# Kernel optimization log

Measured on AMD Instinct MI355X. Metric: run time of the kernel, lower is better.

The kernel has to match this reference:

```python
import jax, jax.numpy as jnp
import numpy as np

N, E = 50000, 800000
IN_F, C, H, OUT_F = 128, 32, 4, 4
HC = H * C
EPS = 1e-5


def gatv2(x, src, dst, ea, Wl, Wr, We, att, bias, concat):
    # x: [N, in], ea: [E, 1], Wl/Wr: [in, H*C], We: [1, H*C], att: [h, C]
    h, c = att.shape
    xl = (x @ Wl).reshape(-1, h, c)          # [N, h, c]
    xr = (x @ Wr).reshape(-1, h, c)          # [N, h, c]
    m = xl[src] + xr[dst] + (ea @ We).reshape(-1, h, c)   # [E, h, c]
    e = jnp.einsum('ehc,hc->eh', jax.nn.leaky_relu(m, 0.2), att)  # [E, h]
    emax = jax.ops.segment_max(e, dst, num_segments=N)
    e = jnp.exp(e - emax[dst])
    denom = jax.ops.segment_sum(e, dst, num_segments=N)
    alpha = e / (denom[dst] + 1e-16)         # [E, h]
    out = jax.ops.segment_sum(alpha[:, :, None] * xl[src], dst, num_segments=N)  # [N, h, c]
    out = out.reshape(N, h * c) if concat else out.mean(axis=1)
    return out + bias


def bn_eval(x, g, b, m, v):
    return (x - m) * jax.lax.rsqrt(v + EPS) * g + b


def setup_inputs() -> dict:
    key = jax.random.key(0)
    ks = iter(jax.random.split(key, 40))
    nrm = lambda shape, s=0.2: jax.random.normal(next(ks), shape, jnp.float32) * s
    d = {}
    d['x'] = jax.random.normal(next(ks), (N, IN_F), jnp.float32)
    d['edge_index'] = jax.random.randint(next(ks), (2, E), 0, N, jnp.int32)
    d['edge_attr'] = jax.random.normal(next(ks), (E, 1), jnp.float32)
    # layer 1
    d['l1_Wl'] = nrm((IN_F, HC)); d['l1_Wr'] = nrm((IN_F, HC))
    d['l1_We'] = nrm((1, HC)); d['l1_att'] = nrm((H, C)); d['l1_b'] = nrm((HC,))
    # layers 2-9 stacked
    d['mid_Wl'] = nrm((8, HC, HC)); d['mid_Wr'] = nrm((8, HC, HC))
    d['mid_We'] = nrm((8, 1, HC)); d['mid_att'] = nrm((8, H, C)); d['mid_b'] = nrm((8, HC))
    # layer 10: heads=1, concat=False
    d['l10_Wl'] = nrm((HC, C)); d['l10_Wr'] = nrm((HC, C))
    d['l10_We'] = nrm((1, C)); d['l10_att'] = nrm((1, C)); d['l10_b'] = nrm((C,))
    # batchnorms (eval mode): bn1-9 stacked, bn10 separate
    d['bn_g'] = jax.random.uniform(next(ks), (9, HC), jnp.float32, 0.5, 1.5)
    d['bn_b'] = nrm((9, HC)); d['bn_m'] = nrm((9, HC))
    d['bn_v'] = jax.random.uniform(next(ks), (9, HC), jnp.float32, 0.5, 1.5)
    d['bn10_g'] = jax.random.uniform(next(ks), (C,), jnp.float32, 0.5, 1.5)
    d['bn10_b'] = nrm((C,)); d['bn10_m'] = nrm((C,))
    d['bn10_v'] = jax.random.uniform(next(ks), (C,), jnp.float32, 0.5, 1.5)
    d['lin_W'] = nrm((C, OUT_F)); d['lin_b'] = nrm((OUT_F,))
    return d


def reference(x, edge_index, edge_attr,
              l1_Wl, l1_Wr, l1_We, l1_att, l1_b,
              mid_Wl, mid_Wr, mid_We, mid_att, mid_b,
              l10_Wl, l10_Wr, l10_We, l10_att, l10_b,
              bn_g, bn_b, bn_m, bn_v,
              bn10_g, bn10_b, bn10_m, bn10_v,
              lin_W, lin_b):
    src, dst = edge_index[0], edge_index[1]
    h = jax.nn.relu(gatv2(x, src, dst, edge_attr, l1_Wl, l1_Wr, l1_We, l1_att, l1_b, True))
    h = bn_eval(h, bn_g[0], bn_b[0], bn_m[0], bn_v[0])
    for i in range(8):  # layers 2-9
        h = jax.nn.relu(gatv2(h, src, dst, edge_attr, mid_Wl[i], mid_Wr[i], mid_We[i], mid_att[i], mid_b[i], True))
        h = bn_eval(h, bn_g[i + 1], bn_b[i + 1], bn_m[i + 1], bn_v[i + 1])
    h = jax.nn.relu(gatv2(h, src, dst, edge_attr, l10_Wl, l10_Wr, l10_We, l10_att, l10_b, False))
    h = bn_eval(h, bn10_g, bn10_b, bn10_m, bn10_v)
    return h @ lin_W + lin_b
```

## Files before the change

kernel.cpp:

```cpp
#include <hip/hip_runtime.h>
#include <math.h>

#define NN 50000
#define EE 800000
#define EPS 1e-5f
#define SCAN_CH 196

#define NEG_BIG (-1e30f)
#define RESCALE_THR 4.0f

#define LO_SCALE 2048.0f
#define LO_INV   (1.0f/2048.0f)

typedef unsigned short u16;
typedef _Float16 f16x8 __attribute__((ext_vector_type(8)));
typedef float f32x4 __attribute__((ext_vector_type(4)));

__device__ __forceinline__ u16 f2h(float f) {
    _Float16 h = (_Float16)f;
    return __builtin_bit_cast(u16, h);
}
__device__ __forceinline__ float h2f(u16 u) {
    return (float)__builtin_bit_cast(_Float16, u);
}

__device__ __forceinline__ float dpp_add8(float x) {
    int t;
    t = __builtin_amdgcn_update_dpp(0, __float_as_int(x), 0xB1, 0xf, 0xf, true);
    x += __int_as_float(t);
    t = __builtin_amdgcn_update_dpp(0, __float_as_int(x), 0x4E, 0xf, 0xf, true);
    x += __int_as_float(t);
    t = __builtin_amdgcn_update_dpp(0, __float_as_int(x), 0x141, 0xf, 0xf, true);
    x += __int_as_float(t);
    return x;
}

__global__ void hist_kernel(const int* __restrict__ dst, int* cnt) {
    int e = blockIdx.x * blockDim.x + threadIdx.x;
    if (e < EE) atomicAdd(&cnt[dst[e]], 1);
}

__global__ void scan_part(const int* __restrict__ cnt, int* __restrict__ part) {
    __shared__ int red[256];
    int b = blockIdx.x, t = threadIdx.x;
    int i = b * SCAN_CH + t;
    int v = (t < SCAN_CH && i < NN) ? cnt[i] : 0;
    red[t] = v;
    __syncthreads();
#pragma unroll
    for (int s = 128; s; s >>= 1) {
        if (t < s) red[t] += red[t + s];
        __syncthreads();
    }
    if (t == 0) part[b] = red[0];
}

__global__ void scan_block(int* part) {
    __shared__ int buf[2][256];
    int t = threadIdx.x;
    int v = part[t];
    int p = 0;
    buf[0][t] = v;
    __syncthreads();
#pragma unroll
    for (int off = 1; off < 256; off <<= 1) {
        buf[p ^ 1][t] = buf[p][t] + ((t >= off) ? buf[p][t - off] : 0);
        __syncthreads();
        p ^= 1;
    }
    part[t] = buf[p][t] - v;
}

__global__ void scan_final(int* __restrict__ cntcur, const int* __restrict__ part,
                           int* __restrict__ row_start) {
    __shared__ int buf[2][256];
    int b = blockIdx.x, t = threadIdx.x;
    int i = b * SCAN_CH + t;
    int v = (t < SCAN_CH && i < NN) ? cntcur[i] : 0;
    int p = 0;
    buf[0][t] = v;
    __syncthreads();
#pragma unroll
    for (int off = 1; off < 256; off <<= 1) {
        buf[p ^ 1][t] = buf[p][t] + ((t >= off) ? buf[p][t - off] : 0);
        __syncthreads();
        p ^= 1;
    }
    if (t < SCAN_CH && i < NN) {
        int pos = part[b] + buf[p][t] - v;
        row_start[i] = pos;
        cntcur[i] = pos;
    }
    if (b == 0 && t == 0) row_start[NN] = EE;
}

__global__ void scatter_kernel(const int* __restrict__ ei, const float* __restrict__ ea,
                               int* cursor, int2* __restrict__ edge_pack) {
    int e = blockIdx.x * blockDim.x + threadIdx.x;
    if (e < EE) {
        int d = ei[EE + e];
        int pos = atomicAdd(&cursor[d], 1);
        edge_pack[pos] = make_int2(ei[e], __float_as_int(ea[e]));
    }
}

__global__ void split_f32(const float* __restrict__ in, u16* __restrict__ hi,
                          u16* __restrict__ lo, int n4) {
    int i = blockIdx.x * blockDim.x + threadIdx.x;
    if (i >= n4) return;
    float4 v = ((const float4*)in)[i];
    ushort4 h, l;
    h.x = f2h(v.x); l.x = f2h((v.x - h2f(h.x)) * LO_SCALE);
    h.y = f2h(v.y); l.y = f2h((v.y - h2f(h.y)) * LO_SCALE);
    h.z = f2h(v.z); l.z = f2h((v.z - h2f(h.z)) * LO_SCALE);
    h.w = f2h(v.w); l.w = f2h((v.w - h2f(h.w)) * LO_SCALE);
    ((ushort4*)hi)[i] = h;
    ((ushort4*)lo)[i] = l;
}

__global__ void conv_w(const float* __restrict__ l1Wl, const float* __restrict__ l1Wr,
                       const float* __restrict__ midWl, const float* __restrict__ midWr,
                       u16* __restrict__ Wh, u16* __restrict__ Wlo) {
    int tid = blockIdx.x * 256 + threadIdx.x;
    if (tid >= 9 * 256 * 128) return;
    int L = tid >> 15;
    int rem = tid & 32767;
    int n = rem >> 7, k = rem & 127;
    const float* WL;
    const float* WR;
    if (L == 0) { WL = l1Wl; WR = l1Wr; }
    else {
        WL = midWl + (size_t)(L - 1) * 16384;
        WR = midWr + (size_t)(L - 1) * 16384;
    }
    float w = (n < 128) ? WL[k * 128 + n] : WR[k * 128 + (n - 128)];
    u16 h = f2h(w);
    Wh[tid] = h;
    Wlo[tid] = f2h((w - h2f(h)) * LO_SCALE);
}

__global__ void conv_w10(const float* __restrict__ Wl, const float* __restrict__ Wr,
                         u16* __restrict__ Wh, u16* __restrict__ Wlo) {
    int tid = blockIdx.x * 256 + threadIdx.x;
    if (tid >= 64 * 128) return;
    int n = tid >> 7, k = tid & 127;
    float w = (n < 32) ? Wl[k * 32 + n] : Wr[k * 32 + (n - 32)];
    u16 h = f2h(w);
    Wh[tid] = h;
    Wlo[tid] = f2h((w - h2f(h)) * LO_SCALE);
}

__global__ __launch_bounds__(256) void gemm_mfma(const u16* __restrict__ Ah,
                                                 const u16* __restrict__ Al,
                                                 const u16* __restrict__ Bh,
                                                 const u16* __restrict__ Bl,
                                                 float* __restrict__ C) {
    int bid = blockIdx.x;
    int jj = bid & 7;
    int y  = (bid >> 3) & 1;
    int x  = (bid >> 4) * 8 + jj;
    if (x >= (NN + 63) / 64) return;

    int w    = threadIdx.x >> 6;
    int lane = threadIdx.x & 63;
    int lr = lane & 15;
    int kg = lane >> 4;
    int rowbase = x * 64;
    int colb = w * 32;
    int colbase = y * 128 + colb;

    f16x8 bh[2][4], bl[2][4];
#pragma unroll
    for (int ct = 0; ct < 2; ++ct) {
        size_t boff = (size_t)(colbase + ct * 16 + lr) * 128 + (size_t)(kg * 8);
#pragma unroll
        for (int ks = 0; ks < 4; ++ks) {
            bh[ct][ks] = *(const f16x8*)(Bh + boff + ks * 32);
            bl[ct][ks] = *(const f16x8*)(Bl + boff + ks * 32);
        }
    }

    auto aoff_of = [&](int rt) {
        int arow = rowbase + rt * 16 + lr;
        if (arow >= NN) arow = NN - 1;
        return (size_t)arow * 128 + (size_t)(kg * 8);
    };
    f16x8 ahc[4], alc[4], ahn[4], aln[4];
    {
        size_t ao = aoff_of(0);
#pragma unroll
        for (int ks = 0; ks < 4; ++ks) {
            ahc[ks] = *(const f16x8*)(Ah + ao + ks * 32);
            alc[ks] = *(const f16x8*)(Al + ao + ks * 32);
        }
    }

    float* Cp = C + (size_t)y * ((size_t)NN * 128);

#pragma unroll
    for (int rt = 0; rt < 4; ++rt) {
        if (rt < 3) {
            size_t ao = aoff_of(rt + 1);
#pragma unroll
            for (int ks = 0; ks < 4; ++ks) {
                ahn[ks] = *(const f16x8*)(Ah + ao + ks * 32);
                aln[ks] = *(const f16x8*)(Al + ao + ks * 32);
            }
        }

        f32x4 aH[2], aL[2];
#pragma unroll
        for (int ct = 0; ct < 2; ++ct) {
            aH[ct] = (f32x4){0.f, 0.f, 0.f, 0.f};
            aL[ct] = (f32x4){0.f, 0.f, 0.f, 0.f};
        }
#pragma unroll
        for (int ks = 0; ks < 4; ++ks) {
#pragma unroll
            for (int ct = 0; ct < 2; ++ct) {
                aH[ct] = __builtin_amdgcn_mfma_f32_16x16x32_f16(ahc[ks], bh[ct][ks], aH[ct], 0, 0, 0);
                aL[ct] = __builtin_amdgcn_mfma_f32_16x16x32_f16(alc[ks], bh[ct][ks], aL[ct], 0, 0, 0);
                aL[ct] = __builtin_amdgcn_mfma_f32_16x16x32_f16(ahc[ks], bl[ct][ks], aL[ct], 0, 0, 0);
            }
        }

        int crow0 = rowbase + rt * 16 + kg * 4;
#pragma unroll
        for (int ct = 0; ct < 2; ++ct) {
            float* cp = Cp + (size_t)crow0 * 128 + colb + ct * 16 + lr;
#pragma unroll
            for (int r = 0; r < 4; ++r) {
                if (crow0 + r < NN)
                    cp[(size_t)r * 128] = fmaf(aL[ct][r], LO_INV, aH[ct][r]);
            }
        }

        if (rt < 3) {
#pragma unroll
            for (int ks = 0; ks < 4; ++ks) { ahc[ks] = ahn[ks]; alc[ks] = aln[ks]; }
        }
    }
}

__global__ __launch_bounds__(256) void gemm_mfma_l10(const u16* __restrict__ Ah,
                                                     const u16* __restrict__ Al,
                                                     const u16* __restrict__ Bh,
                                                     const u16* __restrict__ Bl,
                                                     float* __restrict__ C) {
    int w    = threadIdx.x >> 6;
    int lane = threadIdx.x & 63;
    int lr = lane & 15;
    int kg = lane >> 4;
    int rowbase = blockIdx.x * 64;
    int colb = w * 16;

    f16x8 bh[4], bl[4];
    {
        size_t boff = (size_t)(colb + lr) * 128 + (size_t)(kg * 8);
#pragma unroll
        for (int ks = 0; ks < 4; ++ks) {
            bh[ks] = *(const f16x8*)(Bh + boff + ks * 32);
            bl[ks] = *(const f16x8*)(Bl + boff + ks * 32);
        }
    }

    auto aoff_of = [&](int rt) {
        int arow = rowbase + rt * 16 + lr;
        if (arow >= NN) arow = NN - 1;
        return (size_t)arow * 128 + (size_t)(kg * 8);
    };
    f16x8 ahc[4], alc[4], ahn[4], aln[4];
    {
        size_t ao = aoff_of(0);
#pragma unroll
        for (int ks = 0; ks < 4; ++ks) {
            ahc[ks] = *(const f16x8*)(Ah + ao + ks * 32);
            alc[ks] = *(const f16x8*)(Al + ao + ks * 32);
        }
    }

#pragma unroll
    for (int rt = 0; rt < 4; ++rt) {
        if (rt < 3) {
            size_t ao = aoff_of(rt + 1);
#pragma unroll
            for (int ks = 0; ks < 4; ++ks) {
                ahn[ks] = *(const f16x8*)(Ah + ao + ks * 32);
                aln[ks] = *(const f16x8*)(Al + ao + ks * 32);
            }
        }

        f32x4 aH = (f32x4){0.f, 0.f, 0.f, 0.f};
        f32x4 aL = (f32x4){0.f, 0.f, 0.f, 0.f};
#pragma unroll
        for (int ks = 0; ks < 4; ++ks) {
            aH = __builtin_amdgcn_mfma_f32_16x16x32_f16(ahc[ks], bh[ks], aH, 0, 0, 0);
            aL = __builtin_amdgcn_mfma_f32_16x16x32_f16(alc[ks], bh[ks], aL, 0, 0, 0);
            aL = __builtin_amdgcn_mfma_f32_16x16x32_f16(ahc[ks], bl[ks], aL, 0, 0, 0);
        }

        int crow0 = rowbase + rt * 16 + kg * 4;
        float* cp = C + (size_t)crow0 * 64 + colb + lr;
#pragma unroll
        for (int r = 0; r < 4; ++r) {
            if (crow0 + r < NN)
                cp[(size_t)r * 64] = fmaf(aL[r], LO_INV, aH[r]);
        }

        if (rt < 3) {
#pragma unroll
            for (int ks = 0; ks < 4; ++ks) { ahc[ks] = ahn[ks]; alc[ks] = aln[ks]; }
        }
    }
}

__global__ __launch_bounds__(256) void node_agg_128(const float* __restrict__ xlr,
                                                    const int* __restrict__ row_start,
                                                    const int2* __restrict__ epack,
                                                    const float* __restrict__ We,
                                                    const float* __restrict__ att,
                                                    const float* __restrict__ bias,
                                                    const float* __restrict__ bng,
                                                    const float* __restrict__ bnb,
                                                    const float* __restrict__ bnm,
                                                    const float* __restrict__ bnv,
                                                    u16* __restrict__ ahi,
                                                    u16* __restrict__ alo) {
    int node = (blockIdx.x * blockDim.x + threadIdx.x) >> 6;
    int lane = threadIdx.x & 63;
    if (node >= NN) return;
    int half = lane >> 5;
    int c0   = (lane & 31) << 2;

    const float* xlp = xlr;
    const float* xrp = xlr + (size_t)NN * 128;

    const float L2E = 1.44269504f;
    const float4 xr4 = *(const float4*)(xrp + (size_t)node * 128 + c0);
    const float4 we4 = *(const float4*)(We + c0);
    const float4 at4 = *(const float4*)(att + c0);
    float4 a6, a4;
    a6.x = 0.6f * L2E * at4.x; a4.x = 0.4f * L2E * at4.x;
    a6.y = 0.6f * L2E * at4.y; a4.y = 0.4f * L2E * at4.y;
    a6.z = 0.6f * L2E * at4.z; a4.z = 0.4f * L2E * at4.z;
    a6.w = 0.6f * L2E * at4.w; a4.w = 0.4f * L2E * at4.w;

    int beg = row_start[node], end = row_start[node + 1];
    int lastE = end - 1;

    float mx0 = NEG_BIG, sm0 = 0.f;
    float mx1 = NEG_BIG, sm1 = 0.f;
    float4 ac0 = make_float4(0.f, 0.f, 0.f, 0.f);
    float4 ac1 = make_float4(0.f, 0.f, 0.f, 0.f);

    auto score = [&](float eav, const float4& xv) -> float {
        float m0 = xv.x + fmaf(eav, we4.x, xr4.x);
        float m1 = xv.y + fmaf(eav, we4.y, xr4.y);
        float m2 = xv.z + fmaf(eav, we4.z, xr4.z);
        float m3 = xv.w + fmaf(eav, we4.w, xr4.w);
        float p = fmaf(a6.x, m0, a4.x * fabsf(m0));
        p = fmaf(a6.y, m1, fmaf(a4.y, fabsf(m1), p));
        p = fmaf(a6.z, m2, fmaf(a4.z, fabsf(m2), p));
        p = fmaf(a6.w, m3, fmaf(a4.w, fabsf(m3), p));
        return dpp_add8(p);
    };

    auto upd = [&](float& mx, float& sm, float4& ac, float p, const float4& xv) {
        float d = p - mx;
        if (__ballot(d > RESCALE_THR)) {
            float nm = fmaxf(mx, p);
            float sc = exp2f(mx - nm);
            float w  = exp2f(p - nm);
            sm = fmaf(sm, sc, w);
            ac.x = fmaf(ac.x, sc, w * xv.x);
            ac.y = fmaf(ac.y, sc, w * xv.y);
            ac.z = fmaf(ac.z, sc, w * xv.z);
            ac.w = fmaf(ac.w, sc, w * xv.w);
            mx = nm;
        } else {
            float w = exp2f(d);
            sm += w;
            ac.x = fmaf(w, xv.x, ac.x);
            ac.y = fmaf(w, xv.y, ac.y);
            ac.z = fmaf(w, xv.z, ac.z);
            ac.w = fmaf(w, xv.w, ac.w);
        }
    };

    int j = beg;
    for (; j + 3 < end; j += 4) {
        int2 pkA = epack[j + half];
        int2 pkB = epack[j + 2 + half];
        float4 xA = *(const float4*)(xlp + ((size_t)pkA.x << 7) + c0);
        float4 xB = *(const float4*)(xlp + ((size_t)pkB.x << 7) + c0);
        float pA = score(__int_as_float(pkA.y), xA);
        float pB = score(__int_as_float(pkB.y), xB);
        upd(mx0, sm0, ac0, pA, xA);
        upd(mx1, sm1, ac1, pB, xB);
    }
    if (j < end) {
        int jeA = j + half;       bool dA = jeA > lastE; if (dA) jeA = lastE;
        int jeB = j + 2 + half;   bool dB = jeB > lastE; if (dB) jeB = lastE;
        int2 pkA = epack[jeA];
        int2 pkB = epack[jeB];
        float4 xA = *(const float4*)(xlp + ((size_t)pkA.x << 7) + c0);
        float4 xB = *(const float4*)(xlp + ((size_t)pkB.x << 7) + c0);
        float pA = score(__int_as_float(pkA.y), xA);
        float pB = score(__int_as_float(pkB.y), xB);
        pA = dA ? NEG_BIG : pA;
        pB = dB ? NEG_BIG : pB;
        upd(mx0, sm0, ac0, pA, xA);
        upd(mx1, sm1, ac1, pB, xB);
    }

    float Mx = fmaxf(mx0, mx1);
    float s0 = exp2f(mx0 - Mx), s1 = exp2f(mx1 - Mx);
    float sm = fmaf(sm0, s0, sm1 * s1);
    float4 ac;
    ac.x = fmaf(ac0.x, s0, ac1.x * s1);
    ac.y = fmaf(ac0.y, s0, ac1.y * s1);
    ac.z = fmaf(ac0.z, s0, ac1.z * s1);
    ac.w = fmaf(ac0.w, s0, ac1.w * s1);

    float  Mo  = __shfl_xor(Mx, 32);
    float  smo = __shfl_xor(sm, 32);
    float4 aco;
    aco.x = __shfl_xor(ac.x, 32);
    aco.y = __shfl_xor(ac.y, 32);
    aco.z = __shfl_xor(ac.z, 32);
    aco.w = __shfl_xor(ac.w, 32);
    float Mn = fmaxf(Mx, Mo);
    float ss = exp2f(Mx - Mn), so = exp2f(Mo - Mn);
    sm   = fmaf(sm, ss, smo * so);
    ac.x = fmaf(ac.x, ss, aco.x * so);
    ac.y = fmaf(ac.y, ss, aco.y * so);
    ac.z = fmaf(ac.z, ss, aco.z * so);
    ac.w = fmaf(ac.w, ss, aco.w * so);

    if (half == 0) {
        float inv = 1.f / (sm + 1e-16f);
        const float4 b4  = *(const float4*)(bias + c0);
        const float4 g4  = *(const float4*)(bng + c0);
        const float4 bb4 = *(const float4*)(bnb + c0);
        const float4 m4  = *(const float4*)(bnm + c0);
        const float4 v4  = *(const float4*)(bnv + c0);
        float4 y;
        y.x = fmaxf(fmaf(ac.x, inv, b4.x), 0.f);
        y.y = fmaxf(fmaf(ac.y, inv, b4.y), 0.f);
        y.z = fmaxf(fmaf(ac.z, inv, b4.z), 0.f);
        y.w = fmaxf(fmaf(ac.w, inv, b4.w), 0.f);
        y.x = (y.x - m4.x) * rsqrtf(v4.x + EPS) * g4.x + bb4.x;
        y.y = (y.y - m4.y) * rsqrtf(v4.y + EPS) * g4.y + bb4.y;
        y.z = (y.z - m4.z) * rsqrtf(v4.z + EPS) * g4.z + bb4.z;
        y.w = (y.w - m4.w) * rsqrtf(v4.w + EPS) * g4.w + bb4.w;

        ushort4 hh, ll;
        hh.x = f2h(y.x); ll.x = f2h((y.x - h2f(hh.x)) * LO_SCALE);
        hh.y = f2h(y.y); ll.y = f2h((y.y - h2f(hh.y)) * LO_SCALE);
        hh.z = f2h(y.z); ll.z = f2h((y.z - h2f(hh.z)) * LO_SCALE);
        hh.w = f2h(y.w); ll.w = f2h((y.w - h2f(hh.w)) * LO_SCALE);
        *(ushort4*)(ahi + (size_t)node * 128 + c0) = hh;
        *(ushort4*)(alo + (size_t)node * 128 + c0) = ll;
    }
}

__global__ __launch_bounds__(256) void node_agg_l10(const float* __restrict__ xlr,
                                                    const int* __restrict__ row_start,
                                                    const int2* __restrict__ epack,
                                                    const float* __restrict__ We,
                                                    const float* __restrict__ att,
                                                    const float* __restrict__ bias,
                                                    const float* __restrict__ bng,
                                                    const float* __restrict__ bnb,
                                                    const float* __restrict__ bnm,
                                                    const float* __restrict__ bnv,
                                                    const float* __restrict__ linW,
                                                    const float* __restrict__ linb,
                                                    float* __restrict__ out) {
    int n = (blockIdx.x * blockDim.x + threadIdx.x) >> 5;
    if (n >= NN) return;
    int q    = threadIdx.x & 31;
    int slot = q >> 3;
    int c0   = (q & 7) << 2;

    const float L2E = 1.44269504f;
    const float4 xr = *(const float4*)(xlr + (size_t)n * 64 + 32 + c0);
    const float4 we = *(const float4*)(We + c0);
    const float4 at = *(const float4*)(att + c0);
    float4 a6, a4;
    a6.x = 0.6f * L2E * at.x; a4.x = 0.4f * L2E * at.x;
    a6.y = 0.6f * L2E * at.y; a4.y = 0.4f * L2E * at.y;
    a6.z = 0.6f * L2E * at.z; a4.z = 0.4f * L2E * at.z;
    a6.w = 0.6f * L2E * at.w; a4.w = 0.4f * L2E * at.w;

    int beg = row_start[n], end = row_start[n + 1];
    int lastE = end - 1;

    float mx = NEG_BIG, sm = 0.f;
    float4 ac = make_float4(0.f, 0.f, 0.f, 0.f);

    auto score4 = [&](float eav, const float4& xv) -> float {
        float m0 = xv.x + fmaf(eav, we.x, xr.x);
        float m1 = xv.y + fmaf(eav, we.y, xr.y);
        float m2 = xv.z + fmaf(eav, we.z, xr.z);
        float m3 = xv.w + fmaf(eav, we.w, xr.w);
        float p = fmaf(a6.x, m0, a4.x * fabsf(m0));
        p = fmaf(a6.y, m1, fmaf(a4.y, fabsf(m1), p));
        p = fmaf(a6.z, m2, fmaf(a4.z, fabsf(m2), p));
        p = fmaf(a6.w, m3, fmaf(a4.w, fabsf(m3), p));
        return dpp_add8(p);
    };

    auto upd = [&](float p, const float4& xv) {
        float d = p - mx;
        if (__ballot(d > RESCALE_THR)) {
            float nm = fmaxf(mx, p);
            float sc = exp2f(mx - nm);
            float w  = exp2f(p - nm);
            sm = fmaf(sm, sc, w);
            ac.x = fmaf(ac.x, sc, w * xv.x); ac.y = fmaf(ac.y, sc, w * xv.y);
            ac.z = fmaf(ac.z, sc, w * xv.z); ac.w = fmaf(ac.w, sc, w * xv.w);
            mx = nm;
        } else {
            float w = exp2f(d);
            sm += w;
            ac.x = fmaf(w, xv.x, ac.x); ac.y = fmaf(w, xv.y, ac.y);
            ac.z = fmaf(w, xv.z, ac.z); ac.w = fmaf(w, xv.w, ac.w);
        }
    };

    int nE = end - beg;
    int last4 = beg + (nE & ~3);

    int2 pkn; float4 xvn;
    if (beg < last4) {
        pkn = epack[beg + slot];
        xvn = *(const float4*)(xlr + ((size_t)pkn.x << 6) + c0);
    }
    for (int j = beg; j < last4; ) {
        int2 pk = pkn; float4 xv = xvn;
        j += 4;
        if (j < last4) {
            pkn = epack[j + slot];
            xvn = *(const float4*)(xlr + ((size_t)pkn.x << 6) + c0);
        }
        float p = score4(__int_as_float(pk.y), xv);
        upd(p, xv);
    }
    if (last4 < end) {
        int je = last4 + slot;
        bool dead = je > lastE; if (dead) je = lastE;
        int2 pk = epack[je];
        float4 xv = *(const float4*)(xlr + ((size_t)pk.x << 6) + c0);
        float p = score4(__int_as_float(pk.y), xv);
        p = dead ? NEG_BIG : p;
        upd(p, xv);
    }

#pragma unroll
    for (int off = 8; off <= 16; off <<= 1) {
        float  Mo  = __shfl_xor(mx, off);
        float  smo = __shfl_xor(sm, off);
        float4 aco;
        aco.x = __shfl_xor(ac.x, off); aco.y = __shfl_xor(ac.y, off);
        aco.z = __shfl_xor(ac.z, off); aco.w = __shfl_xor(ac.w, off);
        float Mn = fmaxf(mx, Mo);
        float ss = exp2f(mx - Mn), so = exp2f(Mo - Mn);
        sm = fmaf(sm, ss, smo * so);
        ac.x = fmaf(ac.x, ss, aco.x * so); ac.y = fmaf(ac.y, ss, aco.y * so);
        ac.z = fmaf(ac.z, ss, aco.z * so); ac.w = fmaf(ac.w, ss, aco.w * so);
        mx = Mn;
    }

    float inv = 1.f / (sm + 1e-16f);
    const float4 b4 = *(const float4*)(bias + c0);
    const float4 g4 = *(const float4*)(bng + c0);
    const float4 q4 = *(const float4*)(bnb + c0);
    const float4 m4 = *(const float4*)(bnm + c0);
    const float4 v4 = *(const float4*)(bnv + c0);
    float4 y;
    y.x = fmaxf(fmaf(ac.x, inv, b4.x), 0.f);
    y.y = fmaxf(fmaf(ac.y, inv, b4.y), 0.f);
    y.z = fmaxf(fmaf(ac.z, inv, b4.z), 0.f);
    y.w = fmaxf(fmaf(ac.w, inv, b4.w), 0.f);
    y.x = (y.x - m4.x) * rsqrtf(v4.x + EPS) * g4.x + q4.x;
    y.y = (y.y - m4.y) * rsqrtf(v4.y + EPS) * g4.y + q4.y;
    y.z = (y.z - m4.z) * rsqrtf(v4.z + EPS) * g4.z + q4.z;
    y.w = (y.w - m4.w) * rsqrtf(v4.w + EPS) * g4.w + q4.w;

    const float4 w0 = *(const float4*)(linW + (c0 + 0) * 4);
    const float4 w1 = *(const float4*)(linW + (c0 + 1) * 4);
    const float4 w2 = *(const float4*)(linW + (c0 + 2) * 4);
    const float4 w3 = *(const float4*)(linW + (c0 + 3) * 4);
    float4 t;
    t.x = fmaf(y.x, w0.x, fmaf(y.y, w1.x, fmaf(y.z, w2.x, y.w * w3.x)));
    t.y = fmaf(y.x, w0.y, fmaf(y.y, w1.y, fmaf(y.z, w2.y, y.w * w3.y)));
    t.z = fmaf(y.x, w0.z, fmaf(y.y, w1.z, fmaf(y.z, w2.z, y.w * w3.z)));
    t.w = fmaf(y.x, w0.w, fmaf(y.y, w1.w, fmaf(y.z, w2.w, y.w * w3.w)));
    t.x = dpp_add8(t.x); t.y = dpp_add8(t.y);
    t.z = dpp_add8(t.z); t.w = dpp_add8(t.w);

    if (q == 0) {
        const float4 lb = *(const float4*)linb;
        float4 o;
        o.x = t.x + lb.x; o.y = t.y + lb.y; o.z = t.z + lb.z; o.w = t.w + lb.w;
        *(float4*)(out + (size_t)n * 4) = o;
    }
}

extern "C" void kernel_launch(void* const* d_in, const int* in_sizes, int n_in,
                              void* d_out, int out_size, void* d_ws, size_t ws_size,
                              hipStream_t stream) {
    const float* x      = (const float*)d_in[0];
    const int*   ei     = (const int*)d_in[1];
    const float* ea     = (const float*)d_in[2];
    const float* l1_Wl  = (const float*)d_in[3];
    const float* l1_Wr  = (const float*)d_in[4];
    const float* l1_We  = (const float*)d_in[5];
    const float* l1_att = (const float*)d_in[6];
    const float* l1_b   = (const float*)d_in[7];
    const float* mid_Wl = (const float*)d_in[8];
    const float* mid_Wr = (const float*)d_in[9];
    const float* mid_We = (const float*)d_in[10];
    const float* mid_att= (const float*)d_in[11];
    const float* mid_b  = (const float*)d_in[12];
    const float* l10_Wl = (const float*)d_in[13];
    const float* l10_Wr = (const float*)d_in[14];
    const float* l10_We = (const float*)d_in[15];
    const float* l10_att= (const float*)d_in[16];
    const float* l10_b  = (const float*)d_in[17];
    const float* bn_g   = (const float*)d_in[18];
    const float* bn_b   = (const float*)d_in[19];
    const float* bn_m   = (const float*)d_in[20];
    const float* bn_v   = (const float*)d_in[21];
    const float* bn10_g = (const float*)d_in[22];
    const float* bn10_b = (const float*)d_in[23];
    const float* bn10_m = (const float*)d_in[24];
    const float* bn10_v = (const float*)d_in[25];
    const float* lin_W  = (const float*)d_in[26];
    const float* lin_b  = (const float*)d_in[27];

    char* ws = (char*)d_ws;
    auto take = [&](size_t bytes) { char* p = ws; ws += (bytes + 255) & ~size_t(255); return p; };
    int*   row_start  = (int*)  take(sizeof(int) * (NN + 1));
    int*   cursor     = (int*)  take(sizeof(int) * NN);
    int*   part       = (int*)  take(sizeof(int) * 256);
    int2*  epack      = (int2*) take(sizeof(int2) * EE);
    float* xlr        = (float*)take(sizeof(float) * (size_t)NN * 256);
    u16*   Ahi        = (u16*)  take(sizeof(u16) * (size_t)NN * 128);
    u16*   Alo        = (u16*)  take(sizeof(u16) * (size_t)NN * 128);
    u16*   Wthi       = (u16*)  take(sizeof(u16) * 9 * 256 * 128);
    u16*   Wtlo       = (u16*)  take(sizeof(u16) * 9 * 256 * 128);
    u16*   Wt10hi     = (u16*)  take(sizeof(u16) * 64 * 128);
    u16*   Wt10lo     = (u16*)  take(sizeof(u16) * 64 * 128);

    hipMemsetAsync(cursor, 0, sizeof(int) * NN, stream);
    hist_kernel<<<EE / 256, 256, 0, stream>>>(ei + EE, cursor);
    scan_part<<<256, 256, 0, stream>>>(cursor, part);
    scan_block<<<1, 256, 0, stream>>>(part);
    scan_final<<<256, 256, 0, stream>>>(cursor, part, row_start);
    scatter_kernel<<<EE / 256, 256, 0, stream>>>(ei, ea, cursor, epack);

    split_f32<<<(NN * 128 / 4 + 255) / 256, 256, 0, stream>>>(x, Ahi, Alo, NN * 128 / 4);
    conv_w<<<(9 * 256 * 128 + 255) / 256, 256, 0, stream>>>(l1_Wl, l1_Wr, mid_Wl, mid_Wr,
                                                            Wthi, Wtlo);
    conv_w10<<<(64 * 128 + 255) / 256, 256, 0, stream>>>(l10_Wl, l10_Wr, Wt10hi, Wt10lo);

    const int GBM = (NN + 63) / 64;
    const int GSWZ = ((GBM + 7) / 8) * 16;

    gemm_mfma<<<GSWZ, 256, 0, stream>>>(Ahi, Alo, Wthi, Wtlo, xlr);
    node_agg_128<<<(NN * 64) / 256, 256, 0, stream>>>(
        xlr, row_start, epack, l1_We, l1_att, l1_b,
        bn_g, bn_b, bn_m, bn_v, Ahi, Alo);

    for (int i = 0; i < 8; ++i) {
        gemm_mfma<<<GSWZ, 256, 0, stream>>>(Ahi, Alo,
                                            Wthi + (size_t)(i + 1) * 32768,
                                            Wtlo + (size_t)(i + 1) * 32768, xlr);
        node_agg_128<<<(NN * 64) / 256, 256, 0, stream>>>(
            xlr, row_start, epack,
            mid_We + (size_t)i * 128, mid_att + (size_t)i * 128, mid_b + (size_t)i * 128,
            bn_g + (size_t)(i + 1) * 128, bn_b + (size_t)(i + 1) * 128,
            bn_m + (size_t)(i + 1) * 128, bn_v + (size_t)(i + 1) * 128,
            Ahi, Alo);
    }

    gemm_mfma_l10<<<GBM, 256, 0, stream>>>(Ahi, Alo, Wt10hi, Wt10lo, xlr);
    node_agg_l10<<<(NN * 32 + 255) / 256, 256, 0, stream>>>(
        xlr, row_start, epack, l10_We, l10_att, l10_b,
        bn10_g, bn10_b, bn10_m, bn10_v, lin_W, lin_b, (float*)d_out);
}
```

Measured before the change: 1.212 ms.

## Stage A tile in LDS and cover all 256 output columns per block

```diff
diff --git a/kernel.cpp b/kernel.cpp
--- a/kernel.cpp
+++ b/kernel.cpp
@@ -150,25 +150,26 @@
     Wlo[tid] = f2h((w - h2f(h)) * LO_SCALE);
 }
 
-__global__ __launch_bounds__(256) void gemm_mfma(const u16* __restrict__ Ah,
+#define ASTRIDE 136
+
+__global__ __launch_bounds__(512) void gemm_mfma(const u16* __restrict__ Ah,
                                                  const u16* __restrict__ Al,
                                                  const u16* __restrict__ Bh,
                                                  const u16* __restrict__ Bl,
                                                  float* __restrict__ C) {
-    int bid = blockIdx.x;
-    int jj = bid & 7;
-    int y  = (bid >> 3) & 1;
-    int x  = (bid >> 4) * 8 + jj;
-    if (x >= (NN + 63) / 64) return;
-
-    int w    = threadIdx.x >> 6;
-    int lane = threadIdx.x & 63;
+    __shared__ u16 Ahs[64 * ASTRIDE];
+    __shared__ u16 Als[64 * ASTRIDE];
+
+    int t    = threadIdx.x;
+    int w    = t >> 6;
+    int lane = t & 63;
     int lr = lane & 15;
     int kg = lane >> 4;
-    int rowbase = x * 64;
-    int colb = w * 32;
-    int colbase = y * 128 + colb;
-
+    int rowbase = blockIdx.x * 64;
+
+    int colbase = w * 32;
+    int y    = colbase >> 7;
+    int colb = colbase & 127;
     f16x8 bh[2][4], bl[2][4];
 #pragma unroll
     for (int ct = 0; ct < 2; ++ct) {
@@ -180,32 +181,28 @@
         }
     }
 
-    auto aoff_of = [&](int rt) {
-        int arow = rowbase + rt * 16 + lr;
-        if (arow >= NN) arow = NN - 1;
-        return (size_t)arow * 128 + (size_t)(kg * 8);
-    };
-    f16x8 ahc[4], alc[4], ahn[4], aln[4];
-    {
-        size_t ao = aoff_of(0);
+#pragma unroll
+    for (int i = 0; i < 2; ++i) {
+        int c = t + i * 512;
+        int row  = c >> 4;
+        int colu = (c & 15) * 8;
+        int grow = rowbase + row; if (grow >= NN) grow = NN - 1;
+        size_t go = (size_t)grow * 128 + colu;
+        *(f16x8*)(Ahs + row * ASTRIDE + colu) = *(const f16x8*)(Ah + go);
+        *(f16x8*)(Als + row * ASTRIDE + colu) = *(const f16x8*)(Al + go);
+    }
+    __syncthreads();
+
+    float* Cp = C + (size_t)y * ((size_t)NN * 128);
+
+#pragma unroll
+    for (int rt = 0; rt < 4; ++rt) {
+        int abase = (rt * 16 + lr) * ASTRIDE + kg * 8;
+        f16x8 ah[4], al[4];
 #pragma unroll
         for (int ks = 0; ks < 4; ++ks) {
-            ahc[ks] = *(const f16x8*)(Ah + ao + ks * 32);
-            alc[ks] = *(const f16x8*)(Al + ao + ks * 32);
-        }
-    }
-
-    float* Cp = C + (size_t)y * ((size_t)NN * 128);
-
-#pragma unroll
-    for (int rt = 0; rt < 4; ++rt) {
-        if (rt < 3) {
-            size_t ao = aoff_of(rt + 1);
-#pragma unroll
-            for (int ks = 0; ks < 4; ++ks) {
-                ahn[ks] = *(const f16x8*)(Ah + ao + ks * 32);
-                aln[ks] = *(const f16x8*)(Al + ao + ks * 32);
-            }
+            ah[ks] = *(const f16x8*)(Ahs + abase + ks * 32);
+            al[ks] = *(const f16x8*)(Als + abase + ks * 32);
         }
 
         f32x4 aH[2], aL[2];
@@ -218,9 +215,9 @@
         for (int ks = 0; ks < 4; ++ks) {
 #pragma unroll
             for (int ct = 0; ct < 2; ++ct) {
-                aH[ct] = __builtin_amdgcn_mfma_f32_16x16x32_f16(ahc[ks], bh[ct][ks], aH[ct], 0, 0, 0);
-                aL[ct] = __builtin_amdgcn_mfma_f32_16x16x32_f16(alc[ks], bh[ct][ks], aL[ct], 0, 0, 0);
-                aL[ct] = __builtin_amdgcn_mfma_f32_16x16x32_f16(ahc[ks], bl[ct][ks], aL[ct], 0, 0, 0);
+                aH[ct] = __builtin_amdgcn_mfma_f32_16x16x32_f16(ah[ks], bh[ct][ks], aH[ct], 0, 0, 0);
+                aL[ct] = __builtin_amdgcn_mfma_f32_16x16x32_f16(al[ks], bh[ct][ks], aL[ct], 0, 0, 0);
+                aL[ct] = __builtin_amdgcn_mfma_f32_16x16x32_f16(ah[ks], bl[ct][ks], aL[ct], 0, 0, 0);
             }
         }
 
@@ -233,11 +230,6 @@
                 if (crow0 + r < NN)
                     cp[(size_t)r * 128] = fmaf(aL[ct][r], LO_INV, aH[ct][r]);
             }
-        }
-
-        if (rt < 3) {
-#pragma unroll
-            for (int ks = 0; ks < 4; ++ks) { ahc[ks] = ahn[ks]; alc[ks] = aln[ks]; }
         }
     }
 }
@@ -667,17 +659,16 @@
     conv_w10<<<(64 * 128 + 255) / 256, 256, 0, stream>>>(l10_Wl, l10_Wr, Wt10hi, Wt10lo);
 
     const int GBM = (NN + 63) / 64;
-    const int GSWZ = ((GBM + 7) / 8) * 16;
-
-    gemm_mfma<<<GSWZ, 256, 0, stream>>>(Ahi, Alo, Wthi, Wtlo, xlr);
+
+    gemm_mfma<<<GBM, 512, 0, stream>>>(Ahi, Alo, Wthi, Wtlo, xlr);
     node_agg_128<<<(NN * 64) / 256, 256, 0, stream>>>(
         xlr, row_start, epack, l1_We, l1_att, l1_b,
         bn_g, bn_b, bn_m, bn_v, Ahi, Alo);
 
     for (int i = 0; i < 8; ++i) {
-        gemm_mfma<<<GSWZ, 256, 0, stream>>>(Ahi, Alo,
-                                            Wthi + (size_t)(i + 1) * 32768,
-                                            Wtlo + (size_t)(i + 1) * 32768, xlr);
+        gemm_mfma<<<GBM, 512, 0, stream>>>(Ahi, Alo,
+                                           Wthi + (size_t)(i + 1) * 32768,
+                                           Wtlo + (size_t)(i + 1) * 32768, xlr);
         node_agg_128<<<(NN * 64) / 256, 256, 0, stream>>>(
             xlr, row_start, epack,
             mid_We + (size_t)i * 128, mid_att + (size_t)i * 128, mid_b + (size_t)i * 128,
```

New measurement: 1.053 ms. 13.1% less time.
